# Kernel tuning notes

Measured on AMD Instinct MI355X. Metric: run time of the kernel, lower is better.

## Reference

```python
import jax, jax.numpy as jnp
import numpy as np

C64 = jnp.complex64
N_WIRES = 4


def _rx_b(theta):  # theta: [b] -> [b,2,2]
    c = jnp.cos(theta / 2).astype(C64)
    s = (-1j * jnp.sin(theta / 2)).astype(C64)
    return jnp.stack([jnp.stack([c, s], -1), jnp.stack([s, c], -1)], -2)


def _ry_b(theta):
    c = jnp.cos(theta / 2).astype(C64)
    s = jnp.sin(theta / 2).astype(C64)
    return jnp.stack([jnp.stack([c, -s], -1), jnp.stack([s, c], -1)], -2)


def _rz_b(theta):
    em = jnp.exp(-1j * theta.astype(C64) / 2)
    ep = jnp.exp(1j * theta.astype(C64) / 2)
    z = jnp.zeros_like(em)
    return jnp.stack([jnp.stack([em, z], -1), jnp.stack([z, ep], -1)], -2)


def _crx_mat(theta):  # scalar -> [4,4]
    c = jnp.cos(theta / 2).astype(C64)
    s = (-1j * jnp.sin(theta / 2)).astype(C64)
    m = jnp.eye(4, dtype=C64)
    m = m.at[2, 2].set(c).at[3, 3].set(c).at[2, 3].set(s).at[3, 2].set(s)
    return m


def _apply_1q(state, U, w):
    # state: [b,2,2,2,2]; U: [b,2,2] (batched) or [2,2]
    s = jnp.moveaxis(state, w + 1, 1)
    sh = s.shape
    s = s.reshape(sh[0], 2, -1)
    if U.ndim == 3:
        s = jnp.einsum('bij,bjr->bir', U, s)
    else:
        s = jnp.einsum('ij,bjr->bir', U, s)
    return jnp.moveaxis(s.reshape(sh), 1, w + 1)


def _apply_2q(state, U, wa, wb):
    # state: [b,2,2,2,2]; U: [4,4]; wa = first wire (high bit of U index)
    s = jnp.moveaxis(state, (wa + 1, wb + 1), (1, 2))
    sh = s.shape
    s = s.reshape(sh[0], 4, -1)
    s = jnp.einsum('ij,bjr->bir', U, s)
    return jnp.moveaxis(s.reshape(sh), (1, 2), (wa + 1, wb + 1))


_H = (1.0 / np.sqrt(2.0)) * jnp.array([[1, 1], [1, -1]], dtype=C64)
_SX = 0.5 * jnp.array([[1 + 1j, 1 - 1j], [1 - 1j, 1 + 1j]], dtype=C64)
_CNOT = jnp.array([[1, 0, 0, 0], [0, 1, 0, 0], [0, 0, 0, 1], [0, 0, 1, 0]], dtype=C64)
_U12 = jnp.array([[1, 0, 0, 0], [0, 1, 0, 0], [0, 0, 0, 1j], [0, 0, -1j, 0]], dtype=C64)


def setup_inputs() -> dict:
    key = jax.random.key(0)
    k0, k1, k2, k3, k4 = jax.random.split(key, 5)
    bsz = 131072
    return {
        'x': jax.random.normal(k0, (bsz, 1, 24, 24), dtype=jnp.float32),
        'theta_rx0': jax.random.normal(k1, (1,), dtype=jnp.float32),
        'theta_ry0': jax.random.normal(k2, (1,), dtype=jnp.float32),
        'theta_rz0': jax.random.normal(k3, (1,), dtype=jnp.float32),
        'theta_crx0': jax.random.normal(k4, (1,), dtype=jnp.float32),
    }


def reference(x, theta_rx0, theta_ry0, theta_rz0, theta_crx0):
    b = x.shape[0]
    # avg_pool2d(kernel=6, stride=6) on 24x24 -> 4x4, flatten to 16 angles
    xp = x.reshape(b, 4, 6, 4, 6).mean(axis=(2, 4)).reshape(b, 16)
    # |0000> state
    state = jnp.zeros((b, 2, 2, 2, 2), dtype=C64).at[:, 0, 0, 0, 0].set(1.0)
    # encoder: rx*4, ry*4, rz*4, rx*4 on wires k % 4 with batched angles
    for k in range(4):
        state = _apply_1q(state, _rx_b(xp[:, k]), k)
    for k in range(4):
        state = _apply_1q(state, _ry_b(xp[:, 4 + k]), k)
    for k in range(4):
        state = _apply_1q(state, _rz_b(xp[:, 8 + k]), k)
    for k in range(4):
        state = _apply_1q(state, _rx_b(xp[:, 12 + k]), k)
    # trainable gates (shared scalar params)
    state = _apply_1q(state, _rx_b(theta_rx0)[0], 0)
    state = _apply_1q(state, _ry_b(theta_ry0)[0], 1)
    state = _apply_1q(state, _rz_b(theta_rz0)[0], 3)
    state = _apply_2q(state, _crx_mat(theta_crx0[0]), 0, 2)
    state = _apply_1q(state, _H, 3)
    state = _apply_1q(state, _SX, 2)
    state = _apply_2q(state, _CNOT, 3, 0)
    state = _apply_2q(state, _U12, 1, 2)
    # MeasureAll(PauliZ): <Z_w> per wire
    probs = state.real ** 2 + state.imag ** 2  # [b,2,2,2,2]
    zvals = jnp.array([1.0, -1.0], dtype=probs.dtype)
    exps = []
    for w in range(N_WIRES):
        shape = [1] + [2 if i == w else 1 for i in range(N_WIRES)]
        exps.append((probs * zvals.reshape(shape)).sum(axis=(1, 2, 3, 4)))
    z = jnp.stack(exps, axis=-1)  # [b,4]
    logits = z.reshape(b, 2, 2).sum(-1)  # [b,2]
    return jax.nn.log_softmax(logits, axis=1)
```

## Files before the change

kernel.cpp:

```cpp
#include <hip/hip_runtime.h>


#define CH 8
#define PADF 584
#define XPS 257
#define NCHUNK 32

__device__ __forceinline__ void cmul(float ar, float ai, float br, float bi,
                                     float& cr, float& ci) {
  cr = ar * br - ai * bi;
  ci = ar * bi + ai * br;
}

struct C2 { float r0, i0, r1, i1; };

__device__ __forceinline__ void g_rx(C2& v, float h) {
  float s, c; __sincosf(h, &s, &c);
  C2 n;
  n.r0 = c * v.r0 + s * v.i1;
  n.i0 = c * v.i0 - s * v.r1;
  n.r1 = c * v.r1 + s * v.i0;
  n.i1 = c * v.i1 - s * v.r0;
  v = n;
}
__device__ __forceinline__ void g_ry(C2& v, float h) {
  float s, c; __sincosf(h, &s, &c);
  C2 n;
  n.r0 = c * v.r0 - s * v.r1;
  n.i0 = c * v.i0 - s * v.i1;
  n.r1 = s * v.r0 + c * v.r1;
  n.i1 = s * v.i0 + c * v.i1;
  v = n;
}
__device__ __forceinline__ void g_rz(C2& v, float h) {
  float s, c; __sincosf(h, &s, &c);
  C2 n;
  n.r0 = c * v.r0 + s * v.i0;
  n.i0 = c * v.i0 - s * v.r0;
  n.r1 = c * v.r1 - s * v.i1;
  n.i1 = c * v.i1 + s * v.r1;
  v = n;
}

__global__ __launch_bounds__(256, 2)
void qfc_kernel(const float* __restrict__ x,
                const float* __restrict__ thrx,
                const float* __restrict__ thry,
                const float* __restrict__ thrz,
                const float* __restrict__ thcrx,
                float* __restrict__ out) {
  __shared__ float stage[2][CH * PADF];
  __shared__ float xp[16][XPS];

  const int t = threadIdx.x;
  const long long img0 = (long long)blockIdx.x * 256;
  const float4* __restrict__ x4 = reinterpret_cast<const float4*>(x);

  float4 s0, s1, s2, s3, s4;

  auto load_chunk = [&](int c) {
    long long base = (img0 + (long long)c * CH) * 144;
    s0 = x4[base + (0 * 256 + t)];
    s1 = x4[base + (1 * 256 + t)];
    s2 = x4[base + (2 * 256 + t)];
    s3 = x4[base + (3 * 256 + t)];
    if (t < 128) s4 = x4[base + (4 * 256 + t)];
  };
  auto write_chunk = [&](int buf) {
    float* sp = stage[buf];
    auto wr = [&](int idx, float4 v) {
      int img = idx / 144;
      int off4 = idx - img * 144;
      *reinterpret_cast<float4*>(&sp[img * PADF + off4 * 4]) = v;
    };
    wr(0 * 256 + t, s0);
    wr(1 * 256 + t, s1);
    wr(2 * 256 + t, s2);
    wr(3 * 256 + t, s3);
    if (t < 128) wr(4 * 256 + t, s4);
  };

  load_chunk(0);
  write_chunk(0);
  __syncthreads();

  for (int c = 0; c < NCHUNK; ++c) {
    if (c + 1 < NCHUNK) load_chunk(c + 1);
    if (t < CH * 16) {
      int img = t >> 4;
      int pool = t & 15;
      int r0 = pool >> 2, c0 = pool & 3;
      const float* b = &stage[c & 1][img * PADF + r0 * 144 + c0 * 6];
      float sum = 0.f;
#pragma unroll
      for (int r = 0; r < 6; ++r) {
        float2 a0 = *reinterpret_cast<const float2*>(b + r * 24);
        float2 a1 = *reinterpret_cast<const float2*>(b + r * 24 + 2);
        float2 a2 = *reinterpret_cast<const float2*>(b + r * 24 + 4);
        sum += a0.x + a0.y + a1.x + a1.y + a2.x + a2.y;
      }
      xp[pool][c * CH + img] = sum * (1.0f / 36.0f);
    }
    __syncthreads();
    if (c + 1 < NCHUNK) write_chunk((c + 1) & 1);
    __syncthreads();
  }

  float a[16];
#pragma unroll
  for (int j = 0; j < 16; ++j) a[j] = xp[j][t];

  const float arx = thrx[0] * 0.5f;
  const float ary = thry[0] * 0.5f;
  const float arz = thrz[0] * 0.5f;
  const float acr = thcrx[0] * 0.5f;

  C2 v[4];
#pragma unroll
  for (int w = 0; w < 4; ++w) {
    v[w].r0 = 1.f; v[w].i0 = 0.f; v[w].r1 = 0.f; v[w].i1 = 0.f;
    g_rx(v[w], a[w] * 0.5f);
    g_ry(v[w], a[4 + w] * 0.5f);
    g_rz(v[w], a[8 + w] * 0.5f);
    g_rx(v[w], a[12 + w] * 0.5f);
  }
  g_rx(v[0], arx);
  g_ry(v[1], ary);
  g_rz(v[3], arz);

  float t01r[4], t01i[4], t23r[4], t23i[4];
  cmul(v[0].r0, v[0].i0, v[1].r0, v[1].i0, t01r[0], t01i[0]);
  cmul(v[0].r0, v[0].i0, v[1].r1, v[1].i1, t01r[1], t01i[1]);
  cmul(v[0].r1, v[0].i1, v[1].r0, v[1].i0, t01r[2], t01i[2]);
  cmul(v[0].r1, v[0].i1, v[1].r1, v[1].i1, t01r[3], t01i[3]);
  cmul(v[2].r0, v[2].i0, v[3].r0, v[3].i0, t23r[0], t23i[0]);
  cmul(v[2].r0, v[2].i0, v[3].r1, v[3].i1, t23r[1], t23i[1]);
  cmul(v[2].r1, v[2].i1, v[3].r0, v[3].i0, t23r[2], t23i[2]);
  cmul(v[2].r1, v[2].i1, v[3].r1, v[3].i1, t23r[3], t23i[3]);

  float re[16], im[16];
#pragma unroll
  for (int hi = 0; hi < 4; ++hi)
#pragma unroll
    for (int lo = 0; lo < 4; ++lo)
      cmul(t01r[hi], t01i[hi], t23r[lo], t23i[lo], re[hi * 4 + lo], im[hi * 4 + lo]);

  {
    float s, cc; __sincosf(acr, &s, &cc);
#pragma unroll
    for (int k = 0; k < 4; ++k) {
      const int pi4[4] = {8, 9, 12, 13};
      int i = pi4[k], j = i + 2;
      float nir = cc * re[i] + s * im[j];
      float nii = cc * im[i] - s * re[j];
      float njr = cc * re[j] + s * im[i];
      float nji = cc * im[j] - s * re[i];
      re[i] = nir; im[i] = nii; re[j] = njr; im[j] = nji;
    }
  }
#pragma unroll
  for (int i = 0; i < 16; i += 2) {
    const float inv = 0.70710678118654752f;
    float ar = re[i], ai = im[i], br = re[i + 1], bi = im[i + 1];
    re[i] = (ar + br) * inv;     im[i] = (ai + bi) * inv;
    re[i + 1] = (ar - br) * inv; im[i + 1] = (ai - bi) * inv;
  }
#pragma unroll
  for (int i = 0; i < 16; ++i) {
    if ((i & 2) == 0) {
      int j = i + 2;
      float ar = re[i], ai = im[i], br = re[j], bi = im[j];
      re[i] = 0.5f * (ar - ai + br + bi);
      im[i] = 0.5f * (ar + ai - br + bi);
      re[j] = 0.5f * (ar + ai + br - bi);
      im[j] = 0.5f * (ai - ar + br + bi);
    }
  }
#pragma unroll
  for (int i = 1; i < 8; i += 2) {
    float tr = re[i], ti = im[i];
    re[i] = re[i + 8]; im[i] = im[i + 8];
    re[i + 8] = tr;    im[i + 8] = ti;
  }
#pragma unroll
  for (int k = 0; k < 4; ++k) {
    const int ii4[4] = {4, 5, 12, 13};
    int i = ii4[k], j = i + 2;
    float tr = re[i], ti = im[i];
    re[i] = -im[j]; im[i] = re[j];
    re[j] = ti;     im[j] = -tr;
  }

  float z0 = 0.f, z1 = 0.f, z2 = 0.f, z3 = 0.f;
#pragma unroll
  for (int i = 0; i < 16; ++i) {
    float p = re[i] * re[i] + im[i] * im[i];
    z0 += (i & 8) ? -p : p;
    z1 += (i & 4) ? -p : p;
    z2 += (i & 2) ? -p : p;
    z3 += (i & 1) ? -p : p;
  }
  float l0 = z0 + z1, l1 = z2 + z3;
  float m = fmaxf(l0, l1);
  float e0 = __expf(l0 - m), e1 = __expf(l1 - m);
  float lse = __logf(e0 + e1);
  float2 o;
  o.x = l0 - m - lse;
  o.y = l1 - m - lse;
  reinterpret_cast<float2*>(out)[img0 + t] = o;
}

extern "C" void kernel_launch(void* const* d_in, const int* in_sizes, int n_in,
                              void* d_out, int out_size, void* d_ws, size_t ws_size,
                              hipStream_t stream) {
  const float* x = (const float*)d_in[0];
  const float* thrx = (const float*)d_in[1];
  const float* thry = (const float*)d_in[2];
  const float* thrz = (const float*)d_in[3];
  const float* thcrx = (const float*)d_in[4];
  float* out = (float*)d_out;
  qfc_kernel<<<512, 256, 0, stream>>>(x, thrx, thry, thrz, thcrx, out);
}
```

Measured before the change: 52.10 us.

## Use single-wave blocks with register double-buffered loads and barrier-free pooling

Measured after the change: 131.6 us. 2.53x slower.

```diff
diff --git a/kernel.cpp b/kernel.cpp
--- a/kernel.cpp
+++ b/kernel.cpp
@@ -1,10 +1,5 @@
 #include <hip/hip_runtime.h>
 
-
-#define CH 8
-#define PADF 584
-#define XPS 257
-#define NCHUNK 32
 
 __device__ __forceinline__ void cmul(float ar, float ai, float br, float bi,
                                      float& cr, float& ci) {
@@ -42,73 +37,66 @@
   v = n;
 }
 
-__global__ __launch_bounds__(256, 2)
+#define NC 16
+
+__global__ __launch_bounds__(64, 2)
 void qfc_kernel(const float* __restrict__ x,
                 const float* __restrict__ thrx,
                 const float* __restrict__ thry,
                 const float* __restrict__ thrz,
                 const float* __restrict__ thcrx,
                 float* __restrict__ out) {
-  __shared__ float stage[2][CH * PADF];
-  __shared__ float xp[16][XPS];
-
-  const int t = threadIdx.x;
-  const long long img0 = (long long)blockIdx.x * 256;
-  const float4* __restrict__ x4 = reinterpret_cast<const float4*>(x);
-
-  float4 s0, s1, s2, s3, s4;
-
-  auto load_chunk = [&](int c) {
-    long long base = (img0 + (long long)c * CH) * 144;
-    s0 = x4[base + (0 * 256 + t)];
-    s1 = x4[base + (1 * 256 + t)];
-    s2 = x4[base + (2 * 256 + t)];
-    s3 = x4[base + (3 * 256 + t)];
-    if (t < 128) s4 = x4[base + (4 * 256 + t)];
+  __shared__ float stage[2304];
+  __shared__ float xp[1024];
+
+  const int l = threadIdx.x;
+  const long long img0 = (long long)blockIdx.x * 64;
+  const float4* __restrict__ base4 =
+      reinterpret_cast<const float4*>(x) + img0 * 144;
+
+  float4 rA[9], rB[9];
+
+  auto issue = [&](float4* r, int c) {
+    const int b = c * 576 + l;
+#pragma unroll
+    for (int k = 0; k < 9; ++k) r[k] = base4[b + k * 64];
   };
-  auto write_chunk = [&](int buf) {
-    float* sp = stage[buf];
-    auto wr = [&](int idx, float4 v) {
-      int img = idx / 144;
-      int off4 = idx - img * 144;
-      *reinterpret_cast<float4*>(&sp[img * PADF + off4 * 4]) = v;
-    };
-    wr(0 * 256 + t, s0);
-    wr(1 * 256 + t, s1);
-    wr(2 * 256 + t, s2);
-    wr(3 * 256 + t, s3);
-    if (t < 128) wr(4 * 256 + t, s4);
+  auto put = [&](const float4* r) {
+#pragma unroll
+    for (int k = 0; k < 9; ++k)
+      *reinterpret_cast<float4*>(&stage[(k * 64 + l) * 4]) = r[k];
   };
-
-  load_chunk(0);
-  write_chunk(0);
-  __syncthreads();
-
-  for (int c = 0; c < NCHUNK; ++c) {
-    if (c + 1 < NCHUNK) load_chunk(c + 1);
-    if (t < CH * 16) {
-      int img = t >> 4;
-      int pool = t & 15;
-      int r0 = pool >> 2, c0 = pool & 3;
-      const float* b = &stage[c & 1][img * PADF + r0 * 144 + c0 * 6];
-      float sum = 0.f;
-#pragma unroll
-      for (int r = 0; r < 6; ++r) {
-        float2 a0 = *reinterpret_cast<const float2*>(b + r * 24);
-        float2 a1 = *reinterpret_cast<const float2*>(b + r * 24 + 2);
-        float2 a2 = *reinterpret_cast<const float2*>(b + r * 24 + 4);
-        sum += a0.x + a0.y + a1.x + a1.y + a2.x + a2.y;
-      }
-      xp[pool][c * CH + img] = sum * (1.0f / 36.0f);
+  auto pool = [&](int c) {
+    const int img = l >> 4;
+    const int p = l & 15;
+    const int r0 = p >> 2, c0 = p & 3;
+    const float* b = &stage[img * 576 + r0 * 144 + c0 * 6];
+    float sum = 0.f;
+#pragma unroll
+    for (int r = 0; r < 6; ++r) {
+      float2 a0 = *reinterpret_cast<const float2*>(b + r * 24);
+      float2 a1 = *reinterpret_cast<const float2*>(b + r * 24 + 2);
+      float2 a2 = *reinterpret_cast<const float2*>(b + r * 24 + 4);
+      sum += a0.x + a0.y + a1.x + a1.y + a2.x + a2.y;
     }
-    __syncthreads();
-    if (c + 1 < NCHUNK) write_chunk((c + 1) & 1);
-    __syncthreads();
+    const int col = (c * 4 + img) ^ ((p << 2) & 63);
+    xp[p * 64 + col] = sum * (1.0f / 36.0f);
+  };
+
+  issue(rA, 0);
+  issue(rB, 1);
+  for (int cc = 0; cc < NC; cc += 2) {
+    put(rA);
+    if (cc + 2 < NC) issue(rA, cc + 2);
+    pool(cc);
+    put(rB);
+    if (cc + 3 < NC) issue(rB, cc + 3);
+    pool(cc + 1);
   }
 
   float a[16];
 #pragma unroll
-  for (int j = 0; j < 16; ++j) a[j] = xp[j][t];
+  for (int p = 0; p < 16; ++p) a[p] = xp[p * 64 + (l ^ ((p << 2) & 63))];
 
   const float arx = thrx[0] * 0.5f;
   const float ary = thry[0] * 0.5f;
@@ -146,15 +134,15 @@
       cmul(t01r[hi], t01i[hi], t23r[lo], t23i[lo], re[hi * 4 + lo], im[hi * 4 + lo]);
 
   {
-    float s, cc; __sincosf(acr, &s, &cc);
+    float s, cc2; __sincosf(acr, &s, &cc2);
 #pragma unroll
     for (int k = 0; k < 4; ++k) {
       const int pi4[4] = {8, 9, 12, 13};
       int i = pi4[k], j = i + 2;
-      float nir = cc * re[i] + s * im[j];
-      float nii = cc * im[i] - s * re[j];
-      float njr = cc * re[j] + s * im[i];
-      float nji = cc * im[j] - s * re[i];
+      float nir = cc2 * re[i] + s * im[j];
+      float nii = cc2 * im[i] - s * re[j];
+      float njr = cc2 * re[j] + s * im[i];
+      float nji = cc2 * im[j] - s * re[i];
       re[i] = nir; im[i] = nii; re[j] = njr; im[j] = nji;
     }
   }
@@ -207,7 +195,7 @@
   float2 o;
   o.x = l0 - m - lse;
   o.y = l1 - m - lse;
-  reinterpret_cast<float2*>(out)[img0 + t] = o;
+  reinterpret_cast<float2*>(out)[img0 + l] = o;
 }
 
 extern "C" void kernel_launch(void* const* d_in, const int* in_sizes, int n_in,
@@ -219,5 +207,5 @@
   const float* thrz = (const float*)d_in[3];
   const float* thcrx = (const float*)d_in[4];
   float* out = (float*)d_out;
-  qfc_kernel<<<512, 256, 0, stream>>>(x, thrx, thry, thrz, thcrx, out);
-}
+  qfc_kernel<<<2048, 64, 0, stream>>>(x, thrx, thry, thrz, thcrx, out);
+}
```
